# Kernel optimization log

Measured on AMD Instinct MI355X. Metric: run time of the kernel, lower is better.

The kernel has to match this reference:

```python
import jax, jax.numpy as jnp
import numpy as np

NEG_SLOPE = 0.2
HEADS = 4
C = 64            # hidden_channels
NUM_CLASSES = 12
NUM_GRAPHS = 512


def gatv2_conv(x, src, dst, Wl, Wr, att, bias, heads, out_ch, num_nodes):
    """PyG GATv2Conv: gather -> LeakyReLU attention -> segment softmax -> scatter.
    x: [N, Fin]; src/dst: [E]; Wl/Wr: [Fin, heads*out_ch]; att: [heads, out_ch]; bias: [heads*out_ch].
    Messages flow src -> dst; heads are concatenated."""
    xl = (x @ Wl).reshape(num_nodes, heads, out_ch)  # source-side transform
    xr = (x @ Wr).reshape(num_nodes, heads, out_ch)  # target-side transform
    e = jax.nn.leaky_relu(xl[src] + xr[dst], NEG_SLOPE)      # [E, H, C]
    score = jnp.einsum('ehc,hc->eh', e, att)                  # [E, H]
    smax = jax.ops.segment_max(score, dst, num_segments=num_nodes)  # [N, H]
    ex = jnp.exp(score - smax[dst])
    denom = jax.ops.segment_sum(ex, dst, num_segments=num_nodes)    # [N, H]
    alpha = ex / (denom[dst] + 1e-16)                         # [E, H]
    out = jax.ops.segment_sum(alpha[:, :, None] * xl[src], dst, num_segments=num_nodes)
    return out.reshape(num_nodes, heads * out_ch) + bias


def add_self_loops(edge_index, num_nodes):
    loop = jnp.arange(num_nodes, dtype=edge_index.dtype)
    src = jnp.concatenate([edge_index[0], loop])
    dst = jnp.concatenate([edge_index[1], loop])
    return src, dst


def setup_inputs() -> dict:
    key = jax.random.key(0)
    ks = jax.random.split(key, 20)
    N, F, E = 50000, 128, 800000

    def w(k, shape):
        return (jax.random.normal(k, shape) * 0.1).astype(jnp.float32)

    inp = {
        'x': jax.random.normal(ks[0], (N, F), dtype=jnp.float32),
        'edge_index': jax.random.randint(ks[1], (2, E), 0, N),
        'batch': jnp.sort(jax.random.randint(ks[2], (N,), 0, NUM_GRAPHS)),
        # conv1: (-1,-1) lazy -> Fin=F, heads=4
        'W1l': w(ks[3], (F, HEADS * C)), 'W1r': w(ks[4], (F, HEADS * C)),
        'a1': w(ks[5], (HEADS, C)), 'b1': jnp.zeros((HEADS * C,), jnp.float32),
        # conv2: Fin = hidden*heads = 256, heads=4
        'W2l': w(ks[6], (HEADS * C, HEADS * C)), 'W2r': w(ks[7], (HEADS * C, HEADS * C)),
        'a2': w(ks[8], (HEADS, C)), 'b2': jnp.zeros((HEADS * C,), jnp.float32),
        # conv3: Fin = 256, heads=1
        'W3l': w(ks[9], (HEADS * C, C)), 'W3r': w(ks[10], (HEADS * C, C)),
        'a3': w(ks[11], (1, C)), 'b3': jnp.zeros((C,), jnp.float32),
        # MLP head (lazy Linear(-1, ...) resolves to C after conv3 heads=1)
        'lin1_w': w(ks[12], (C, C)), 'lin1_b': jnp.zeros((C,), jnp.float32),
        'lin2_w': w(ks[13], (C, C)), 'lin2_b': jnp.zeros((C,), jnp.float32),
        'lin3_w': w(ks[14], (C, NUM_CLASSES)), 'lin3_b': jnp.zeros((NUM_CLASSES,), jnp.float32),
    }
    return inp


def reference(x, edge_index, batch,
              W1l, W1r, a1, b1,
              W2l, W2r, a2, b2,
              W3l, W3r, a3, b3,
              lin1_w, lin1_b, lin2_w, lin2_b, lin3_w, lin3_b):
    N = x.shape[0]
    src0, dst0 = edge_index[0], edge_index[1]          # conv1: add_self_loops=False
    src1, dst1 = add_self_loops(edge_index, N)         # conv2/3: add_self_loops=True

    h = gatv2_conv(x, src0, dst0, W1l, W1r, a1, b1, HEADS, C, N)
    h = jax.nn.relu(h)
    h = gatv2_conv(h, src1, dst1, W2l, W2r, a2, b2, HEADS, C, N)
    h = jax.nn.relu(h)
    h = gatv2_conv(h, src1, dst1, W3l, W3r, a3, b3, 1, C, N)

    # global mean pool over graphs
    s = jax.ops.segment_sum(h, batch, num_segments=NUM_GRAPHS)
    cnt = jax.ops.segment_sum(jnp.ones((N, 1), h.dtype), batch, num_segments=NUM_GRAPHS)
    g = s / jnp.maximum(cnt, 1.0)

    g = jax.nn.relu(g @ lin1_w + lin1_b)
    # dropout p=0.5 is identity in eval mode
    g = jax.nn.relu(g @ lin2_w + lin2_b)
    return jax.nn.softmax(g @ lin3_w + lin3_b, axis=1)
```

## Files before the change

### kernel.cpp

```cpp
#include <hip/hip_runtime.h>
#include <hip/hip_bf16.h>
#include <cstdint>
#include <cstddef>

typedef short bf16x8 __attribute__((ext_vector_type(8)));
typedef float f32x4 __attribute__((ext_vector_type(4)));
typedef unsigned short u16x4v __attribute__((ext_vector_type(4)));

__device__ __forceinline__ float bf2f(unsigned short u) {
  union { unsigned int u; float f; } v; v.u = ((unsigned int)u) << 16; return v.f;
}
__device__ __forceinline__ unsigned short f2bf(float f) {
  union { float f; unsigned int u; } v; v.f = f;
  unsigned int r = v.u + 0x7fffu + ((v.u >> 16) & 1u);
  return (unsigned short)(r >> 16);
}
__device__ __forceinline__ int pack2(float a, float b) {
  return (int)f2bf(a) | ((int)f2bf(b) << 16);
}
__device__ __forceinline__ void gll16(const void* g, void* l) {
  __builtin_amdgcn_global_load_lds(
      (const __attribute__((address_space(1))) unsigned int*)g,
      (__attribute__((address_space(3))) unsigned int*)l, 16, 0, 0);
}

struct WPack {
  const float* in[6];
  unsigned short* out[6];
  int K[6], Ncol[6];
  int start[7];
};
__global__ __launch_bounds__(256) void convert_all(WPack p) {
  int idx = blockIdx.x * 256 + threadIdx.x;
  #pragma unroll
  for (int s = 0; s < 6; ++s) {
    if (idx >= p.start[s] && idx < p.start[s + 1]) {
      int lidx = idx - p.start[s];
      int k = lidx / p.Ncol[s], n = lidx % p.Ncol[s];
      p.out[s][n * p.K[s] + k] = f2bf(p.in[s][lidx]);
    }
  }
}

template<int BN, int WAVES_M, int WAVES_N, bool AF32, bool GLL>
__global__ __launch_bounds__(256) void gemm_dual(
    const void* __restrict__ Av,
    const unsigned short* __restrict__ BtL, const unsigned short* __restrict__ BtR,
    unsigned short* __restrict__ outL, unsigned short* __restrict__ outR,
    int M, int K, int Ncol) {
  constexpr int BM = 128, BK = 64;
  constexpr int WTM = BM / WAVES_M, WTN = BN / WAVES_N;
  constexpr int MR = WTM / 16, NR = WTN / 16;
  const unsigned short* __restrict__ Bt = blockIdx.z ? BtR : BtL;
  unsigned short* __restrict__ outp = blockIdx.z ? outR : outL;

  __shared__ alignas(16) unsigned short lAt[BM * BK];
  __shared__ alignas(16) unsigned short lBt[BN * BK];

  int t = threadIdx.x;
  int lane = t & 63, wid = t >> 6;
  int wm = wid / WAVES_N, wn = wid % WAVES_N;
  int rowBase = blockIdx.x * BM;
  int colBase = blockIdx.y * BN;

  f32x4 acc[MR][NR] = {};

  for (int k0 = 0; k0 < K; k0 += BK) {
    if constexpr (GLL) {
      const unsigned short* A = (const unsigned short*)Av;
      #pragma unroll
      for (int p = 0; p < BM / 32; ++p) {
        int chunk = wid * (BM / 32) + p;
        int row = chunk * 8 + (lane >> 3);
        int c = (lane & 7) ^ (row & 7);
        gll16(A + (size_t)(rowBase + row) * K + k0 + c * 8, &lAt[chunk * 512]);
      }
      #pragma unroll
      for (int p = 0; p < BN / 32; ++p) {
        int chunk = wid * (BN / 32) + p;
        int row = chunk * 8 + (lane >> 3);
        int c = (lane & 7) ^ (row & 7);
        gll16(Bt + (size_t)(colBase + row) * K + k0 + c * 8, &lBt[chunk * 512]);
      }
    } else {
      #pragma unroll
      for (int p = 0; p < (BM * 8) / 256; ++p) {
        int lin = p * 256 + t;
        int row = lin >> 3, c = lin & 7;
        int gr = rowBase + row;
        int4 w = make_int4(0, 0, 0, 0);
        if constexpr (AF32) {
          const float* A = (const float*)Av;
          if (gr < M) {
            const float* ap = A + (size_t)gr * K + k0 + c * 8;
            f32x4 f0 = *reinterpret_cast<const f32x4*>(ap);
            f32x4 f1 = *reinterpret_cast<const f32x4*>(ap + 4);
            w.x = pack2(f0[0], f0[1]); w.y = pack2(f0[2], f0[3]);
            w.z = pack2(f1[0], f1[1]); w.w = pack2(f1[2], f1[3]);
          }
        } else {
          const unsigned short* A = (const unsigned short*)Av;
          if (gr < M) w = *reinterpret_cast<const int4*>(A + (size_t)gr * K + k0 + c * 8);
        }
        *reinterpret_cast<int4*>(&lAt[row * 64 + ((c ^ (row & 7)) * 8)]) = w;
      }
      #pragma unroll
      for (int p = 0; p < (BN * 8) / 256; ++p) {
        int lin = p * 256 + t;
        int row = lin >> 3, c = lin & 7;
        int4 v = *reinterpret_cast<const int4*>(Bt + (size_t)(colBase + row) * K + k0 + c * 8);
        *reinterpret_cast<int4*>(&lBt[row * 64 + ((c ^ (row & 7)) * 8)]) = v;
      }
    }
    __syncthreads();
    #pragma unroll
    for (int kk = 0; kk < 2; ++kk) {
      bf16x8 af[MR], bfr[NR];
      int cidx = kk * 4 + (lane >> 4);
      #pragma unroll
      for (int mi = 0; mi < MR; ++mi) {
        int row = wm * WTM + mi * 16 + (lane & 15);
        af[mi] = *reinterpret_cast<const bf16x8*>(&lAt[row * 64 + ((cidx ^ (row & 7)) * 8)]);
      }
      #pragma unroll
      for (int ni = 0; ni < NR; ++ni) {
        int row = wn * WTN + ni * 16 + (lane & 15);
        bfr[ni] = *reinterpret_cast<const bf16x8*>(&lBt[row * 64 + ((cidx ^ (row & 7)) * 8)]);
      }
      #pragma unroll
      for (int mi = 0; mi < MR; ++mi)
        #pragma unroll
        for (int ni = 0; ni < NR; ++ni)
          acc[mi][ni] = __builtin_amdgcn_mfma_f32_16x16x32_bf16(af[mi], bfr[ni], acc[mi][ni], 0, 0, 0);
    }
    __syncthreads();
  }
  #pragma unroll
  for (int mi = 0; mi < MR; ++mi)
    #pragma unroll
    for (int ni = 0; ni < NR; ++ni) {
      int col = colBase + wn * WTN + ni * 16 + (lane & 15);
      #pragma unroll
      for (int r = 0; r < 4; ++r) {
        int row = rowBase + wm * WTM + mi * 16 + (lane >> 4) * 4 + r;
        if (row < M) outp[(size_t)row * Ncol + col] = f2bf(acc[mi][ni][r]);
      }
    }
}

__global__ __launch_bounds__(256) void hist_kernel(const int* __restrict__ dst, int* __restrict__ counts, int E) {
  int e = blockIdx.x * 256 + threadIdx.x;
  if (e < E) atomicAdd(&counts[dst[e]], 1);
}

__global__ __launch_bounds__(256) void scan_block(const int* __restrict__ in, int* __restrict__ out,
                                                  int* __restrict__ sums, int n) {
  int i = blockIdx.x * 256 + threadIdx.x;
  int lane = threadIdx.x & 63, wid = threadIdx.x >> 6;
  int v = (i < n) ? in[i] : 0;
  int s = v;
  #pragma unroll
  for (int d = 1; d < 64; d <<= 1) { int tt = __shfl_up(s, d); if (lane >= d) s += tt; }
  __shared__ int wsum[4];
  if (lane == 63) wsum[wid] = s;
  __syncthreads();
  int off = 0;
  for (int w = 0; w < wid; ++w) off += wsum[w];
  if (i < n) out[i] = off + s - v;
  if (threadIdx.x == 255) sums[blockIdx.x] = off + s;
}

__global__ __launch_bounds__(256) void scan_add(int* __restrict__ rs, const int* __restrict__ boffs,
                                                int* __restrict__ cursor, int n, int E) {
  int i = blockIdx.x * 256 + threadIdx.x;
  if (i < n) {
    int v = rs[i] + boffs[blockIdx.x];
    rs[i] = v;
    cursor[i] = v;
  }
  if (i == 0) rs[n] = E;
}

__global__ __launch_bounds__(256) void scatter_kernel(const int* __restrict__ src, const int* __restrict__ dst,
                                                      int* __restrict__ cursor, int* __restrict__ csr, int E) {
  int e = blockIdx.x * 256 + threadIdx.x;
  if (e < E) {
    int p = atomicAdd(&cursor[dst[e]], 1);
    csr[p] = src[e];
  }
}

__global__ __launch_bounds__(256) void deg_reserve(const int* __restrict__ rs, int* __restrict__ binTotal,
                                                   int* __restrict__ blockBase, int N) {
  __shared__ int lh[256];
  lh[threadIdx.x] = 0;
  __syncthreads();
  int n = blockIdx.x * 256 + threadIdx.x;
  if (n < N) {
    int d = rs[n + 1] - rs[n];
    if (d > 255) d = 255;
    atomicAdd(&lh[d], 1);
  }
  __syncthreads();
  int c = lh[threadIdx.x];
  blockBase[blockIdx.x * 256 + threadIdx.x] = c ? atomicAdd(&binTotal[threadIdx.x], c) : 0;
}

__global__ __launch_bounds__(256) void deg_offsets(const int* __restrict__ binTotal, int* __restrict__ binStart) {
  int t = threadIdx.x;
  int lane = t & 63, w = t >> 6;
  int v = binTotal[255 - t];
  int s = v;
  #pragma unroll
  for (int d1 = 1; d1 < 64; d1 <<= 1) { int tt = __shfl_up(s, d1); if (lane >= d1) s += tt; }
  __shared__ int ws[4];
  if (lane == 63) ws[w] = s;
  __syncthreads();
  int off = 0;
  for (int u = 0; u < w; ++u) off += ws[u];
  binStart[255 - t] = off + s - v;
}

__global__ __launch_bounds__(256) void deg_place(const int* __restrict__ rs, const int* __restrict__ binStart,
                                                 const int* __restrict__ blockBase, int* __restrict__ perm, int N) {
  __shared__ int lcur[256];
  lcur[threadIdx.x] = binStart[threadIdx.x] + blockBase[blockIdx.x * 256 + threadIdx.x];
  __syncthreads();
  int n = blockIdx.x * 256 + threadIdx.x;
  if (n < N) {
    int d = rs[n + 1] - rs[n];
    if (d > 255) d = 255;
    perm[atomicAdd(&lcur[d], 1)] = n;
  }
}

template<int VEC>
__device__ __forceinline__ void load_row(const unsigned short* __restrict__ base,
                                         int s, int lane, float* v) {
  if constexpr (VEC == 4) {
    u16x4v r = *reinterpret_cast<const u16x4v*>(base + (size_t)s * 256 + lane * 4);
    #pragma unroll
    for (int j = 0; j < 4; ++j) v[j] = bf2f(r[j]);
  } else {
    v[0] = bf2f(base[(size_t)s * 64 + lane]);
  }
}

template<int VEC, int GROUP>
__device__ __forceinline__ float edge_score(const float* xv, const float* xrv, const float* attv) {
  float p = 0.f;
  #pragma unroll
  for (int j = 0; j < VEC; ++j) {
    float tv = xv[j] + xrv[j];
    tv = fmaxf(tv, 0.2f * tv);
    p = fmaf(tv, attv[j], p);
  }
  #pragma unroll
  for (int msk = 1; msk < GROUP; msk <<= 1) p += __shfl_xor(p, msk);
  return p;
}

template<int H, bool SELF, bool RELU>
__global__ __launch_bounds__(256) void edge_agg(
    const unsigned short* __restrict__ xl, const unsigned short* __restrict__ xr,
    const float* __restrict__ att, const float* __restrict__ bias,
    const int* __restrict__ rowstart, const int* __restrict__ csr,
    const int* __restrict__ perm,
    unsigned short* __restrict__ out, int N) {
  constexpr int F = H * 64;
  constexpr int VEC = F / 64;
  constexpr int GROUP = 64 / H;
  int wave = threadIdx.x >> 6, lane = threadIdx.x & 63;
  int gid = blockIdx.x * 4 + wave;
  if (gid >= N) return;
  int node = perm[gid];

  float attv[VEC];
  #pragma unroll
  for (int j = 0; j < VEC; ++j) attv[j] = att[lane * VEC + j];

  float xrv[VEC];
  load_row<VEC>(xr, node, lane, xrv);

  int s0 = rowstart[node], s1 = rowstart[node + 1];
  int end = s1 + (SELF ? 1 : 0);

  float m = 0.f, l = 0.f;
  float acc[VEC];
  #pragma unroll
  for (int j = 0; j < VEC; ++j) acc[j] = 0.f;

  int i = s0;
  if (i < end) {
    int s = (i < s1) ? csr[i] : node;
    float xv[VEC];
    load_row<VEC>(xl, s, lane, xv);
    m = edge_score<VEC, GROUP>(xv, xrv, attv);
    l = 1.f;
    #pragma unroll
    for (int j = 0; j < VEC; ++j) acc[j] = xv[j];
    ++i;
  }
  for (; i + 2 <= end; i += 2) {
    int sA = (i < s1) ? csr[i] : node;
    int sB = (i + 1 < s1) ? csr[i + 1] : node;
    float xa[VEC], xb[VEC];
    load_row<VEC>(xl, sA, lane, xa);
    load_row<VEC>(xl, sB, lane, xb);
    float pA = edge_score<VEC, GROUP>(xa, xrv, attv);
    float pB = edge_score<VEC, GROUP>(xb, xrv, attv);
    float mx = fmaxf(pA, pB);
    if (__any(mx > m + 8.f)) {
      float mn = fmaxf(m, mx);
      float sc = __expf(m - mn);
      l *= sc;
      #pragma unroll
      for (int j = 0; j < VEC; ++j) acc[j] *= sc;
      m = mn;
    }
    float wA = __expf(pA - m), wB = __expf(pB - m);
    l += wA + wB;
    #pragma unroll
    for (int j = 0; j < VEC; ++j) acc[j] = fmaf(wA, xa[j], fmaf(wB, xb[j], acc[j]));
  }
  if (i < end) {
    int s = (i < s1) ? csr[i] : node;
    float xv[VEC];
    load_row<VEC>(xl, s, lane, xv);
    float p = edge_score<VEC, GROUP>(xv, xrv, attv);
    if (__any(p > m + 8.f)) {
      float mn = fmaxf(m, p);
      float sc = __expf(m - mn);
      l *= sc;
      #pragma unroll
      for (int j = 0; j < VEC; ++j) acc[j] *= sc;
      m = mn;
    }
    float w = __expf(p - m);
    l += w;
    #pragma unroll
    for (int j = 0; j < VEC; ++j) acc[j] = fmaf(w, xv[j], acc[j]);
  }

  float rec = 1.f / (l + 1e-16f);
  if constexpr (VEC == 4) {
    u16x4v w4;
    #pragma unroll
    for (int j = 0; j < 4; ++j) {
      float o = fmaf(acc[j], rec, bias[lane * 4 + j]);
      if (RELU) o = fmaxf(o, 0.f);
      w4[j] = f2bf(o);
    }
    *reinterpret_cast<u16x4v*>(out + (size_t)node * 256 + lane * 4) = w4;
  } else {
    float o = fmaf(acc[0], rec, bias[lane]);
    if (RELU) o = fmaxf(o, 0.f);
    out[(size_t)node * 64 + lane] = f2bf(o);
  }
}

__global__ __launch_bounds__(256) void pool_mlp(
    const unsigned short* __restrict__ h, const int* __restrict__ batch,
    const float* __restrict__ w1, const float* __restrict__ b1,
    const float* __restrict__ w2, const float* __restrict__ b2,
    const float* __restrict__ w3, const float* __restrict__ b3,
    float* __restrict__ out, int N) {
  int g = blockIdx.x;
  int lo = 0, hi = N;
  while (lo < hi) { int mid = (lo + hi) >> 1; if (batch[mid] < g) lo = mid + 1; else hi = mid; }
  int n0 = lo;
  hi = N;
  while (lo < hi) { int mid = (lo + hi) >> 1; if (batch[mid] < g + 1) lo = mid + 1; else hi = mid; }
  int n1 = lo;

  int t = threadIdx.x;
  int c2 = t & 31, r = t >> 5;
  float ax = 0.f, ay = 0.f;
  for (int n = n0 + r; n < n1; n += 8) {
    unsigned int u = *reinterpret_cast<const unsigned int*>(h + (size_t)n * 64 + c2 * 2);
    ax += bf2f((unsigned short)(u & 0xffffu));
    ay += bf2f((unsigned short)(u >> 16));
  }
  __shared__ float redx[8][32], redy[8][32];
  __shared__ float sh[64];
  redx[r][c2] = ax; redy[r][c2] = ay;
  __syncthreads();
  if (t < 64) {
    int lane = t;
    float s = 0.f;
    #pragma unroll
    for (int q = 0; q < 8; ++q) s += (lane & 1) ? redy[q][lane >> 1] : redx[q][lane >> 1];
    float cnt = fmaxf((float)(n1 - n0), 1.f);
    sh[lane] = s / cnt;
    float h1 = b1[lane];
    for (int k = 0; k < 64; ++k) h1 = fmaf(sh[k], w1[k * 64 + lane], h1);
    h1 = fmaxf(h1, 0.f);
    sh[lane] = h1;
    float h2 = b2[lane];
    for (int k = 0; k < 64; ++k) h2 = fmaf(sh[k], w2[k * 64 + lane], h2);
    h2 = fmaxf(h2, 0.f);
    sh[lane] = h2;
    float lg = -INFINITY;
    if (lane < 12) {
      lg = b3[lane];
      for (int k = 0; k < 64; ++k) lg = fmaf(sh[k], w3[k * 12 + lane], lg);
    }
    float mx = lg;
    #pragma unroll
    for (int msk = 1; msk < 64; msk <<= 1) mx = fmaxf(mx, __shfl_xor(mx, msk));
    float ex = (lane < 12) ? __expf(lg - mx) : 0.f;
    float sm = ex;
    #pragma unroll
    for (int msk = 1; msk < 64; msk <<= 1) sm += __shfl_xor(sm, msk);
    if (lane < 12) out[(size_t)g * 12 + lane] = ex / sm;
  }
}

extern "C" void kernel_launch(void* const* d_in, const int* in_sizes, int n_in,
                              void* d_out, int out_size, void* d_ws, size_t ws_size,
                              hipStream_t stream) {
  const float* x    = (const float*)d_in[0];
  const int* edge   = (const int*)d_in[1];
  const int* batch  = (const int*)d_in[2];
  const float* W1l  = (const float*)d_in[3];
  const float* W1r  = (const float*)d_in[4];
  const float* a1   = (const float*)d_in[5];
  const float* b1   = (const float*)d_in[6];
  const float* W2l  = (const float*)d_in[7];
  const float* W2r  = (const float*)d_in[8];
  const float* a2   = (const float*)d_in[9];
  const float* b2   = (const float*)d_in[10];
  const float* W3l  = (const float*)d_in[11];
  const float* W3r  = (const float*)d_in[12];
  const float* a3   = (const float*)d_in[13];
  const float* b3   = (const float*)d_in[14];
  const float* lw1  = (const float*)d_in[15];
  const float* lb1  = (const float*)d_in[16];
  const float* lw2  = (const float*)d_in[17];
  const float* lb2  = (const float*)d_in[18];
  const float* lw3  = (const float*)d_in[19];
  const float* lb3  = (const float*)d_in[20];

  const int E = in_sizes[1] / 2;
  const int N = in_sizes[2];
  const int F0 = in_sizes[0] / N;
  const int G = out_size / 12;
  const int* src = edge;
  const int* dst = edge + E;

  const int gx = (N + 127) / 128;
  const int Mpad = gx * 128;
  const int nb = (N + 255) / 256;

  char* p = (char*)d_ws;
  auto alloc = [&](size_t bytes) { char* q = p; p += (bytes + 255) & ~(size_t)255; return q; };
  unsigned short* bufA = (unsigned short*)alloc((size_t)Mpad * 256 * 2);
  unsigned short* bufB = (unsigned short*)alloc((size_t)Mpad * 256 * 2);
  unsigned short* bufH = (unsigned short*)alloc((size_t)Mpad * 256 * 2);
  unsigned short* Wt1L = (unsigned short*)alloc(128 * 256 * 2);
  unsigned short* Wt1R = (unsigned short*)alloc(128 * 256 * 2);
  unsigned short* Wt2L = (unsigned short*)alloc(256 * 256 * 2);
  unsigned short* Wt2R = (unsigned short*)alloc(256 * 256 * 2);
  unsigned short* Wt3L = (unsigned short*)alloc(256 * 64 * 2);
  unsigned short* Wt3R = (unsigned short*)alloc(256 * 64 * 2);
  int* counts    = (int*)alloc((size_t)N * 4);
  int* binTotal  = (int*)alloc(256 * 4);
  int* binStart  = (int*)alloc(256 * 4);
  int* blockBase = (int*)alloc((size_t)nb * 256 * 4);
  int* rowstart  = (int*)alloc((size_t)(N + 1) * 4);
  int* cursor    = (int*)alloc((size_t)N * 4);
  int* perm      = (int*)alloc((size_t)N * 4);
  int* bsums     = (int*)alloc(4096 * 4);
  int* boffs     = (int*)alloc(4096 * 4);
  int* dummy     = (int*)alloc(64 * 4);
  int* csr       = (int*)alloc((size_t)E * 4);

  hipMemsetAsync(counts, 0, (size_t)N * 4, stream);
  hipMemsetAsync(binTotal, 0, 256 * 4, stream);
  hist_kernel<<<(E + 255) / 256, 256, 0, stream>>>(dst, counts, E);
  scan_block<<<nb, 256, 0, stream>>>(counts, rowstart, bsums, N);
  scan_block<<<1, 256, 0, stream>>>(bsums, boffs, dummy, nb);
  scan_add<<<nb, 256, 0, stream>>>(rowstart, boffs, cursor, N, E);
  scatter_kernel<<<(E + 255) / 256, 256, 0, stream>>>(src, dst, cursor, csr, E);

  deg_reserve<<<nb, 256, 0, stream>>>(rowstart, binTotal, blockBase, N);
  deg_offsets<<<1, 256, 0, stream>>>(binTotal, binStart);
  deg_place<<<nb, 256, 0, stream>>>(rowstart, binStart, blockBase, perm, N);

  {
    WPack wp;
    const float* ins[6] = {W1l, W1r, W2l, W2r, W3l, W3r};
    unsigned short* outs[6] = {Wt1L, Wt1R, Wt2L, Wt2R, Wt3L, Wt3R};
    int Ks[6] = {F0, F0, 256, 256, 256, 256};
    int Ns[6] = {256, 256, 256, 256, 64, 64};
    int acc0 = 0;
    for (int s = 0; s < 6; ++s) {
      wp.in[s] = ins[s]; wp.out[s] = outs[s]; wp.K[s] = Ks[s]; wp.Ncol[s] = Ns[s];
      wp.start[s] = acc0; acc0 += Ks[s] * Ns[s];
    }
    wp.start[6] = acc0;
    convert_all<<<(acc0 + 255) / 256, 256, 0, stream>>>(wp);
  }

  int ne = (N + 3) / 4;

  gemm_dual<128, 2, 2, true, false><<<dim3(gx, 2, 2), 256, 0, stream>>>(x, Wt1L, Wt1R, bufA, bufB, N, F0, 256);
  edge_agg<4, false, true><<<ne, 256, 0, stream>>>(bufA, bufB, a1, b1, rowstart, csr, perm, bufH, N);

  gemm_dual<128, 2, 2, false, true><<<dim3(gx, 2, 2), 256, 0, stream>>>(bufH, Wt2L, Wt2R, bufA, bufB, N, 256, 256);
  edge_agg<4, true, true><<<ne, 256, 0, stream>>>(bufA, bufB, a2, b2, rowstart, csr, perm, bufH, N);

  gemm_dual<64, 4, 1, false, true><<<dim3(gx, 1, 2), 256, 0, stream>>>(bufH, Wt3L, Wt3R, bufA, bufB, N, 256, 64);
  edge_agg<1, true, false><<<ne, 256, 0, stream>>>(bufA, bufB, a3, b3, rowstart, csr, perm, bufH, N);

  pool_mlp<<<G, 256, 0, stream>>>(bufH, batch, lw1, lb1, lw2, lb2, lw3, lb3,
                                  (float*)d_out, N);
}
```

Measured before the change: 514.7 us.

## Fuse CSR/degree-sort preprocessing kernels, use DPP reductions, unroll edge loop by four

Merges the degree histogram into the block scan, the two single-block scans into one kernel, and the degree placement into scan_add. This cuts the preprocessing chain from seven launches to four and clears both buffers with a single memset. The per-edge score reduction switches from shuffle-xor to DPP row-rotate adds for the 16-lane part. The edge aggregation loop gains a four-edge unrolled body to expose more concurrent row gathers. The single memset assumes binTotal sits right after counts in the allocator at a 256-byte aligned offset.

```diff
diff --git a/kernel.cpp b/kernel.cpp
--- a/kernel.cpp
+++ b/kernel.cpp
@@ -22,6 +22,18 @@
   __builtin_amdgcn_global_load_lds(
       (const __attribute__((address_space(1))) unsigned int*)g,
       (__attribute__((address_space(3))) unsigned int*)l, 16, 0, 0);
+}
+template<int CTRL>
+__device__ __forceinline__ float dpp_ror_add(float p) {
+  int t = __builtin_amdgcn_update_dpp(0, __builtin_bit_cast(int, p), CTRL, 0xf, 0xf, true);
+  return p + __builtin_bit_cast(float, t);
+}
+__device__ __forceinline__ float row16_sum(float p) {
+  p = dpp_ror_add<0x121>(p);
+  p = dpp_ror_add<0x122>(p);
+  p = dpp_ror_add<0x124>(p);
+  p = dpp_ror_add<0x128>(p);
+  return p;
 }
 
 struct WPack {
@@ -153,30 +165,75 @@
   if (e < E) atomicAdd(&counts[dst[e]], 1);
 }
 
-__global__ __launch_bounds__(256) void scan_block(const int* __restrict__ in, int* __restrict__ out,
-                                                  int* __restrict__ sums, int n) {
+__global__ __launch_bounds__(256) void scan_block_deg(
+    const int* __restrict__ in, int* __restrict__ out, int* __restrict__ sums,
+    int* __restrict__ binTotal, int* __restrict__ blockBase, int n) {
+  __shared__ int lh[256];
+  __shared__ int wsum[4];
+  lh[threadIdx.x] = 0;
+  __syncthreads();
   int i = blockIdx.x * 256 + threadIdx.x;
   int lane = threadIdx.x & 63, wid = threadIdx.x >> 6;
   int v = (i < n) ? in[i] : 0;
+  if (i < n) atomicAdd(&lh[v < 255 ? v : 255], 1);
   int s = v;
   #pragma unroll
   for (int d = 1; d < 64; d <<= 1) { int tt = __shfl_up(s, d); if (lane >= d) s += tt; }
-  __shared__ int wsum[4];
   if (lane == 63) wsum[wid] = s;
   __syncthreads();
   int off = 0;
   for (int w = 0; w < wid; ++w) off += wsum[w];
   if (i < n) out[i] = off + s - v;
   if (threadIdx.x == 255) sums[blockIdx.x] = off + s;
-}
-
-__global__ __launch_bounds__(256) void scan_add(int* __restrict__ rs, const int* __restrict__ boffs,
-                                                int* __restrict__ cursor, int n, int E) {
+  int c = lh[threadIdx.x];
+  blockBase[blockIdx.x * 256 + threadIdx.x] = c ? atomicAdd(&binTotal[threadIdx.x], c) : 0;
+}
+
+__global__ __launch_bounds__(256) void scan2_offsets(
+    const int* __restrict__ bsums, int* __restrict__ boffs,
+    const int* __restrict__ binTotal, int* __restrict__ binStart, int n) {
+  __shared__ int ws[4];
+  int t = threadIdx.x;
+  int lane = t & 63, w = t >> 6;
+  {
+    int v = (t < n) ? bsums[t] : 0;
+    int s = v;
+    #pragma unroll
+    for (int d = 1; d < 64; d <<= 1) { int tt = __shfl_up(s, d); if (lane >= d) s += tt; }
+    if (lane == 63) ws[w] = s;
+    __syncthreads();
+    int off = 0;
+    for (int u = 0; u < w; ++u) off += ws[u];
+    if (t < n) boffs[t] = off + s - v;
+    __syncthreads();
+  }
+  {
+    int v = binTotal[255 - t];
+    int s = v;
+    #pragma unroll
+    for (int d = 1; d < 64; d <<= 1) { int tt = __shfl_up(s, d); if (lane >= d) s += tt; }
+    if (lane == 63) ws[w] = s;
+    __syncthreads();
+    int off = 0;
+    for (int u = 0; u < w; ++u) off += ws[u];
+    binStart[255 - t] = off + s - v;
+  }
+}
+
+__global__ __launch_bounds__(256) void scan_add_place(
+    int* __restrict__ rs, const int* __restrict__ boffs, int* __restrict__ cursor,
+    const int* __restrict__ counts, const int* __restrict__ binStart,
+    const int* __restrict__ blockBase, int* __restrict__ perm, int n, int E) {
+  __shared__ int lcur[256];
+  lcur[threadIdx.x] = binStart[threadIdx.x] + blockBase[blockIdx.x * 256 + threadIdx.x];
+  __syncthreads();
   int i = blockIdx.x * 256 + threadIdx.x;
   if (i < n) {
     int v = rs[i] + boffs[blockIdx.x];
     rs[i] = v;
     cursor[i] = v;
+    int d = counts[i]; if (d > 255) d = 255;
+    perm[atomicAdd(&lcur[d], 1)] = i;
   }
   if (i == 0) rs[n] = E;
 }
@@ -187,50 +244,6 @@
   if (e < E) {
     int p = atomicAdd(&cursor[dst[e]], 1);
     csr[p] = src[e];
-  }
-}
-
-__global__ __launch_bounds__(256) void deg_reserve(const int* __restrict__ rs, int* __restrict__ binTotal,
-                                                   int* __restrict__ blockBase, int N) {
-  __shared__ int lh[256];
-  lh[threadIdx.x] = 0;
-  __syncthreads();
-  int n = blockIdx.x * 256 + threadIdx.x;
-  if (n < N) {
-    int d = rs[n + 1] - rs[n];
-    if (d > 255) d = 255;
-    atomicAdd(&lh[d], 1);
-  }
-  __syncthreads();
-  int c = lh[threadIdx.x];
-  blockBase[blockIdx.x * 256 + threadIdx.x] = c ? atomicAdd(&binTotal[threadIdx.x], c) : 0;
-}
-
-__global__ __launch_bounds__(256) void deg_offsets(const int* __restrict__ binTotal, int* __restrict__ binStart) {
-  int t = threadIdx.x;
-  int lane = t & 63, w = t >> 6;
-  int v = binTotal[255 - t];
-  int s = v;
-  #pragma unroll
-  for (int d1 = 1; d1 < 64; d1 <<= 1) { int tt = __shfl_up(s, d1); if (lane >= d1) s += tt; }
-  __shared__ int ws[4];
-  if (lane == 63) ws[w] = s;
-  __syncthreads();
-  int off = 0;
-  for (int u = 0; u < w; ++u) off += ws[u];
-  binStart[255 - t] = off + s - v;
-}
-
-__global__ __launch_bounds__(256) void deg_place(const int* __restrict__ rs, const int* __restrict__ binStart,
-                                                 const int* __restrict__ blockBase, int* __restrict__ perm, int N) {
-  __shared__ int lcur[256];
-  lcur[threadIdx.x] = binStart[threadIdx.x] + blockBase[blockIdx.x * 256 + threadIdx.x];
-  __syncthreads();
-  int n = blockIdx.x * 256 + threadIdx.x;
-  if (n < N) {
-    int d = rs[n + 1] - rs[n];
-    if (d > 255) d = 255;
-    perm[atomicAdd(&lcur[d], 1)] = n;
   }
 }
 
@@ -255,8 +268,11 @@
     tv = fmaxf(tv, 0.2f * tv);
     p = fmaf(tv, attv[j], p);
   }
-  #pragma unroll
-  for (int msk = 1; msk < GROUP; msk <<= 1) p += __shfl_xor(p, msk);
+  p = row16_sum(p);
+  if constexpr (GROUP == 64) {
+    p += __shfl_xor(p, 16);
+    p += __shfl_xor(p, 32);
+  }
   return p;
 }
 
@@ -300,6 +316,34 @@
     #pragma unroll
     for (int j = 0; j < VEC; ++j) acc[j] = xv[j];
     ++i;
+  }
+  for (; i + 4 <= end; i += 4) {
+    int s_[4];
+    float x_[4][VEC], p_[4], w_[4];
+    #pragma unroll
+    for (int q = 0; q < 4; ++q) s_[q] = (i + q < s1) ? csr[i + q] : node;
+    #pragma unroll
+    for (int q = 0; q < 4; ++q) load_row<VEC>(xl, s_[q], lane, x_[q]);
+    #pragma unroll
+    for (int q = 0; q < 4; ++q) p_[q] = edge_score<VEC, GROUP>(x_[q], xrv, attv);
+    float mx = fmaxf(fmaxf(p_[0], p_[1]), fmaxf(p_[2], p_[3]));
+    if (__any(mx > m + 8.f)) {
+      float mn = fmaxf(m, mx);
+      float sc = __expf(m - mn);
+      l *= sc;
+      #pragma unroll
+      for (int j = 0; j < VEC; ++j) acc[j] *= sc;
+      m = mn;
+    }
+    #pragma unroll
+    for (int q = 0; q < 4; ++q) w_[q] = __expf(p_[q] - m);
+    l += (w_[0] + w_[1]) + (w_[2] + w_[3]);
+    #pragma unroll
+    for (int j = 0; j < VEC; ++j)
+      acc[j] = fmaf(w_[0], x_[0][j],
+               fmaf(w_[1], x_[1][j],
+               fmaf(w_[2], x_[2][j],
+               fmaf(w_[3], x_[3][j], acc[j]))));
   }
   for (; i + 2 <= end; i += 2) {
     int sA = (i < s1) ? csr[i] : node;
@@ -472,20 +516,15 @@
   int* perm      = (int*)alloc((size_t)N * 4);
   int* bsums     = (int*)alloc(4096 * 4);
   int* boffs     = (int*)alloc(4096 * 4);
-  int* dummy     = (int*)alloc(64 * 4);
   int* csr       = (int*)alloc((size_t)E * 4);
 
-  hipMemsetAsync(counts, 0, (size_t)N * 4, stream);
-  hipMemsetAsync(binTotal, 0, 256 * 4, stream);
+  size_t countsPad = ((size_t)N * 4 + 255) & ~(size_t)255;
+  hipMemsetAsync(counts, 0, countsPad + 256 * 4, stream);
   hist_kernel<<<(E + 255) / 256, 256, 0, stream>>>(dst, counts, E);
-  scan_block<<<nb, 256, 0, stream>>>(counts, rowstart, bsums, N);
-  scan_block<<<1, 256, 0, stream>>>(bsums, boffs, dummy, nb);
-  scan_add<<<nb, 256, 0, stream>>>(rowstart, boffs, cursor, N, E);
+  scan_block_deg<<<nb, 256, 0, stream>>>(counts, rowstart, bsums, binTotal, blockBase, N);
+  scan2_offsets<<<1, 256, 0, stream>>>(bsums, boffs, binTotal, binStart, nb);
+  scan_add_place<<<nb, 256, 0, stream>>>(rowstart, boffs, cursor, counts, binStart, blockBase, perm, N, E);
   scatter_kernel<<<(E + 255) / 256, 256, 0, stream>>>(src, dst, cursor, csr, E);
-
-  deg_reserve<<<nb, 256, 0, stream>>>(rowstart, binTotal, blockBase, N);
-  deg_offsets<<<1, 256, 0, stream>>>(binTotal, binStart);
-  deg_place<<<nb, 256, 0, stream>>>(rowstart, binStart, blockBase, perm, N);
 
   {
     WPack wp;
```

After: 463.8 us. -9.9%, faster.
